# Performance work log

Measured on AMD Instinct MI355X. Metric: run time of the kernel, lower is better.

## Reference

```python
import jax, jax.numpy as jnp
import numpy as np

N, A, AD, D, H, KTOP = 5, 900, 8, 256, 8, 300


def _bbox_min_max(anchor):
    # anchor: [N,A,8] = x,y,z,logw,logl,logh,sin_yaw,cos_yaw
    xyz = anchor[..., :3]
    w, l, h = [jnp.exp(anchor[..., i]) for i in (3, 4, 5)]
    sy, cy = anchor[..., 6], anchor[..., 7]
    yaw = jnp.arctan2(sy, cy)
    ca, sa = jnp.abs(jnp.cos(yaw)), jnp.abs(jnp.sin(yaw))
    ex = 0.5 * (l * ca + w * sa)
    ey = 0.5 * (l * sa + w * ca)
    half = jnp.stack([ex, ey, 0.5 * h], axis=-1)
    return xyz - half, xyz + half


def _forward(i2j_anchor, b_anchor, b_feature, transform_matrix, anchor_embed,
             w_roi, b_roi, bn_g, bn_b, fc1_w, fc1_b, fc2_w, fc2_b,
             anc_w, anc_b, lam_w, lam_b, wq, bq, wk, bk, wv, bv, wo, bo,
             ln_g, ln_b, K):
    n, a, ad = b_anchor.shape
    d = b_feature.shape[-1]
    heads = lam_w.shape[-1]
    dh = d // heads
    # ROI scoring + topk selection of anchors to broadcast to neighbors
    roi = jax.nn.sigmoid(b_feature @ w_roi + b_roi)[..., 0]              # [N,A]
    top_scores, top_idx = jax.lax.top_k(roi, K)                          # [N,K]
    conf = top_scores > 0.5                                              # [N,K]
    nbr = jnp.take_along_axis(b_feature, top_idx[..., None], axis=1)     # [N,K,D]
    idx4 = jnp.broadcast_to(top_idx[None, :, :, None], (n, n, K, ad))
    i2j_sel = jnp.take_along_axis(i2j_anchor, idx4, axis=2)              # [N,N,K,AD]
    # remove self (eye-mask): off-diagonal j per row i, row-major order
    offdiag = np.array([[j for j in range(n) if j != i] for i in range(n)])
    rows = np.arange(n)[:, None]
    m = K * (n - 1)
    i2j_rm = i2j_sel[rows, offdiag].reshape(n, m, ad)                    # [N,M,AD]
    tm_rm = transform_matrix[rows, offdiag]                              # [N,N-1,4,4]
    key_feat = nbr[offdiag].reshape(n, m, d)                             # [N,M,D]
    conf_rm = conf[offdiag].reshape(n, m, 1)
    nf_masked = key_feat * conf_rm
    # bbox-range masked aggregation of neighbor features into ego anchors
    mn, mx = _bbox_min_max(b_anchor)                                     # [N,A,3]
    centers = i2j_rm[..., :3]                                            # [N,M,3]
    inside = jnp.all((centers[:, None, :, :] >= mn[:, :, None, :]) &
                     (centers[:, None, :, :] <= mx[:, :, None, :]), axis=-1)  # [N,A,M]
    agg = jnp.einsum('nam,nmd->nad', inside.astype(b_feature.dtype), nf_masked)
    is_greater_than_range = ~jnp.any(inside, axis=1)                     # [N,M]
    b_feature = b_feature + agg
    # transform-matrix encoding: first 3 rows of 4x4 -> BN -> MLP
    mlp_in = tm_rm[:, :, :3, :].reshape(-1, 12)
    mu = mlp_in.mean(0)
    var = mlp_in.var(0)
    xbn = (mlp_in - mu) / jnp.sqrt(var + 1e-5) * bn_g + bn_b
    t = jax.nn.relu(xbn @ fc1_w + fc1_b) @ fc2_w + fc2_b                 # [N*(N-1),D]
    trans_enc = jnp.repeat(t.reshape(n, n - 1, 1, d), K, axis=2).reshape(n, m, d)
    key_pos = i2j_rm @ anc_w + anc_b + trans_enc                         # anchorencoder + trans
    # distance-biased attention mask
    diff = b_anchor[:, :, None, :2] - i2j_rm[:, None, :, :2]
    dist = jnp.sqrt(jnp.sum(diff * diff, axis=-1) + 1e-12)               # cdist [N,A,M]
    lm = (b_feature @ lam_w + lam_b).transpose(0, 2, 1)                  # [N,H,A]
    bias = -jnp.log1p(dist)[:, None, :, :] * lm[..., None]               # [N,H,A,M]
    # multi-head attention (query=b_feature(+anchor_embed pos), key/value=neighbors)
    q = b_feature + anchor_embed
    k = key_feat + key_pos
    v = key_feat
    qh = (q @ wq + bq).reshape(n, a, heads, dh)
    kh = (k @ wk + bk).reshape(n, m, heads, dh)
    vh = (v @ wv + bv).reshape(n, m, heads, dh)
    logits = jnp.einsum('nahd,nmhd->nham', qh, kh) / np.sqrt(dh).astype(np.float32) + bias
    attn = jax.nn.softmax(logits, axis=-1)
    out = jnp.einsum('nham,nmhd->nahd', attn, vh).reshape(n, a, d) @ wo + bo
    res = b_feature + out                                                # residual (identity=query)
    mu2 = res.mean(-1, keepdims=True)
    var2 = res.var(-1, keepdims=True)
    return (res - mu2) / jnp.sqrt(var2 + 1e-5) * ln_g + ln_b


def setup_inputs() -> dict:
    key = jax.random.key(0)
    ks = jax.random.split(key, 24)
    s = 0.05
    inp = {
        'i2j_anchor': jax.random.normal(ks[0], (N, N, A, AD), jnp.float32),
        'b_anchor': jax.random.normal(ks[1], (N, A, AD), jnp.float32),
        'b_feature': jax.random.normal(ks[2], (N, A, D), jnp.float32),
        'transform_matrix': jax.random.normal(ks[3], (N, N, 4, 4), jnp.float32),
        'anchor_embed': jax.random.normal(ks[4], (N, A, D), jnp.float32),
        'w_roi': jax.random.normal(ks[5], (D, 1), jnp.float32) * s,
        'b_roi': jnp.zeros((1,), jnp.float32),
        'bn_g': jnp.ones((12,), jnp.float32),
        'bn_b': jnp.zeros((12,), jnp.float32),
        'fc1_w': jax.random.normal(ks[6], (12, D), jnp.float32) * s,
        'fc1_b': jnp.zeros((D,), jnp.float32),
        'fc2_w': jax.random.normal(ks[7], (D, D), jnp.float32) * s,
        'fc2_b': jnp.zeros((D,), jnp.float32),
        'anc_w': jax.random.normal(ks[8], (AD, D), jnp.float32) * s,
        'anc_b': jnp.zeros((D,), jnp.float32),
        'lam_w': jax.random.normal(ks[9], (D, H), jnp.float32) * s,
        'lam_b': jnp.zeros((H,), jnp.float32),
        'wq': jax.random.normal(ks[10], (D, D), jnp.float32) * s,
        'bq': jnp.zeros((D,), jnp.float32),
        'wk': jax.random.normal(ks[11], (D, D), jnp.float32) * s,
        'bk': jnp.zeros((D,), jnp.float32),
        'wv': jax.random.normal(ks[12], (D, D), jnp.float32) * s,
        'bv': jnp.zeros((D,), jnp.float32),
        'wo': jax.random.normal(ks[13], (D, D), jnp.float32) * s,
        'bo': jnp.zeros((D,), jnp.float32),
        'ln_g': jnp.ones((D,), jnp.float32),
        'ln_b': jnp.zeros((D,), jnp.float32),
        'K': KTOP,
    }
    return inp


def reference(i2j_anchor, b_anchor, b_feature, transform_matrix, anchor_embed,
              w_roi, b_roi, bn_g, bn_b, fc1_w, fc1_b, fc2_w, fc2_b,
              anc_w, anc_b, lam_w, lam_b, wq, bq, wk, bk, wv, bv, wo, bo,
              ln_g, ln_b, K):
    return _forward(i2j_anchor, b_anchor, b_feature, transform_matrix, anchor_embed,
                    w_roi, b_roi, bn_g, bn_b, fc1_w, fc1_b, fc2_w, fc2_b,
                    anc_w, anc_b, lam_w, lam_b, wq, bq, wk, bk, wv, bv, wo, bo,
                    ln_g, ln_b, K)
```

## Files before the change

### kernel.cpp

```cpp
#include <hip/hip_runtime.h>
#include <math.h>

#define N_ 5
#define A_ 900
#define AD_ 8
#define D_ 256
#define H_ 8
#define DH_ 32
#define K_ 300
#define NM1_ 4
#define M_ 1200
#define MP_ 1216
#define KC_ 64
#define HALF_ 600
#define NCHUNK2_ 10

typedef _Float16 f16x8 __attribute__((ext_vector_type(8)));
typedef _Float16 f16x4 __attribute__((ext_vector_type(4)));
typedef float f32x4 __attribute__((ext_vector_type(4)));

#define LOG2E_ 1.4426950408889634f

__global__ __launch_bounds__(256) void score_kernel(const float* __restrict__ bf,
                                                    const float* __restrict__ w,
                                                    const float* __restrict__ b,
                                                    float* __restrict__ scores) {
  int wid = threadIdx.x >> 6, lane = threadIdx.x & 63;
  int row = blockIdx.x * 4 + wid;
  if (row >= N_ * A_) return;
  const float* x = bf + (long)row * D_;
  float dot = 0.f;
#pragma unroll
  for (int t = 0; t < 4; t++) dot += x[lane + 64 * t] * w[lane + 64 * t];
#pragma unroll
  for (int o = 32; o; o >>= 1) dot += __shfl_xor(dot, o, 64);
  if (lane == 0) scores[row] = 1.0f / (1.0f + expf(-(dot + b[0])));
}

__global__ __launch_bounds__(1024) void topk_kernel(const float* __restrict__ scores,
                                                    int* __restrict__ top_idx,
                                                    float* __restrict__ conf) {
  __shared__ float sc[1024];
  __shared__ int si[1024];
  int i = blockIdx.x, t = threadIdx.x;
  sc[t] = (t < A_) ? scores[i * A_ + t] : -INFINITY;
  si[t] = t;
  __syncthreads();
  for (int k = 2; k <= 1024; k <<= 1) {
    for (int j = k >> 1; j > 0; j >>= 1) {
      int ixj = t ^ j;
      if (ixj > t) {
        bool dir = ((t & k) == 0);
        float a = sc[t], b = sc[ixj];
        bool sw = dir ? (a < b) : (a > b);
        if (sw) {
          sc[t] = b; sc[ixj] = a;
          int tmp = si[t]; si[t] = si[ixj]; si[ixj] = tmp;
        }
      }
      __syncthreads();
    }
  }
  if (t < K_) {
    top_idx[i * K_ + t] = si[t];
    conf[i * K_ + t] = sc[t] > 0.5f ? 1.0f : 0.0f;
  }
}

__global__ __launch_bounds__(256) void mlp_kernel(const float* __restrict__ tm,
                                                  const float* __restrict__ bn_g, const float* __restrict__ bn_b,
                                                  const float* __restrict__ fc1_w, const float* __restrict__ fc1_b,
                                                  const float* __restrict__ fc2_w, const float* __restrict__ fc2_b,
                                                  float* __restrict__ t_out) {
  int r = blockIdx.x;
  int t = threadIdx.x;
  __shared__ float x[20][12];
  __shared__ float y[12];
  __shared__ float hbuf[D_];
  if (t < 240) {
    int rr = t / 12, f = t % 12;
    int i = rr / NM1_, jj = rr % NM1_;
    int j = jj < i ? jj : jj + 1;
    int r4 = f / 4, c4 = f % 4;
    x[rr][f] = tm[((long)(i * N_ + j) * 4 + r4) * 4 + c4];
  }
  __syncthreads();
  if (t < 12) {
    float s = 0.f;
    for (int rr = 0; rr < 20; rr++) s += x[rr][t];
    float m = s / 20.0f;
    float v = 0.f;
    for (int rr = 0; rr < 20; rr++) { float d = x[rr][t] - m; v += d * d; }
    v /= 20.0f;
    y[t] = (x[r][t] - m) * rsqrtf(v + 1e-5f) * bn_g[t] + bn_b[t];
  }
  __syncthreads();
  float acc = fc1_b[t];
#pragma unroll
  for (int f = 0; f < 12; f++) acc += y[f] * fc1_w[f * D_ + t];
  hbuf[t] = fmaxf(acc, 0.0f);
  __syncthreads();
  float acc2 = fc2_b[t];
  for (int k = 0; k < D_; k++) acc2 += hbuf[k] * fc2_w[k * D_ + t];
  t_out[r * D_ + t] = acc2;
}

#define GKT_ 10
__global__ __launch_bounds__(256) void gather_kernel(const float* __restrict__ b_feature,
                                                     const float* __restrict__ i2j_anchor,
                                                     const int* __restrict__ top_idx,
                                                     const float* __restrict__ conf,
                                                     const float* __restrict__ anc_w,
                                                     const float* __restrict__ anc_b,
                                                     const float* __restrict__ t_mlp,
                                                     _Float16* __restrict__ key_feat16,
                                                     float* __restrict__ conf_rm,
                                                     float* __restrict__ i2j_rm,
                                                     _Float16* __restrict__ key_in16) {
  int blk = blockIdx.x;
  int i = blk / NM1_, jj = blk % NM1_;
  int j = jj < i ? jj : jj + 1;
  int k0 = blockIdx.y * GKT_;
  int c = threadIdx.x;
  __shared__ float aw[AD_][D_];
#pragma unroll
  for (int r = 0; r < AD_; r++) aw[r][c] = anc_w[r * D_ + c];
  float ab = anc_b[c];
  float tv = t_mlp[(i * NM1_ + jj) * D_ + c];
  __syncthreads();
  for (int k = k0; k < k0 + GKT_; k++) {
    int idx = top_idx[j * K_ + k];
    float cf = conf[j * K_ + k];
    const float* src = b_feature + ((long)(j * A_ + idx)) * D_;
    float val = src[c];
    long mrow = (long)i * M_ + jj * K_ + k;
    key_feat16[mrow * D_ + c] = (_Float16)val;
    const float* ap = i2j_anchor + ((long)((i * N_ + j) * A_ + idx)) * AD_;
    if (c < AD_) i2j_rm[mrow * AD_ + c] = ap[c];
    if (c == 0) conf_rm[mrow] = cf;
    float pos = ab + tv;
#pragma unroll
    for (int r = 0; r < AD_; r++) pos += ap[r] * aw[r][c];
    key_in16[mrow * D_ + c] = (_Float16)(val + pos);
  }
}

__global__ __launch_bounds__(256) void trans_kernel(const float* __restrict__ w0, const float* __restrict__ w1,
                                                    const float* __restrict__ w2, const float* __restrict__ w3,
                                                    const _Float16* __restrict__ kf,
                                                    _Float16* __restrict__ wT, _Float16* __restrict__ kT) {
  int bid = blockIdx.x;
  int t = threadIdx.x;
  if (bid < 64) {
    int y = bid >> 4, tile = bid & 15;
    const float* src = (y == 0) ? w0 : (y == 1) ? w1 : (y == 2) ? w2 : w3;
    _Float16* dst = wT + (size_t)y * D_ * D_;
    int kr = (tile >> 2) * 64, nc = (tile & 3) * 64;
    __shared__ float lds[64][65];
#pragma unroll
    for (int r = 0; r < 16; r++) {
      int row = r * 4 + (t >> 6), col = t & 63;
      lds[row][col] = src[(size_t)(kr + row) * D_ + nc + col];
    }
    __syncthreads();
#pragma unroll
    for (int r = 0; r < 16; r++) {
      int orow = r * 4 + (t >> 6), ocol = t & 63;
      dst[(size_t)(nc + orow) * D_ + kr + ocol] = (_Float16)lds[ocol][orow];
    }
  } else {
    int b = bid - 64;
    int i = b / 76, rem = b % 76;
    int m0 = (rem % 19) * 64, d0 = (rem / 19) * 64;
    __shared__ _Float16 lds2[64][66];
    const _Float16* src = kf + (size_t)i * M_ * D_;
    _Float16* dst = kT + (size_t)i * D_ * M_;
#pragma unroll
    for (int r = 0; r < 16; r++) {
      int row = r * 4 + (t >> 6), col = t & 63;
      int m = m0 + row;
      lds2[row][col] = (m < M_) ? src[(size_t)m * D_ + d0 + col] : (_Float16)0.0f;
    }
    __syncthreads();
#pragma unroll
    for (int r = 0; r < 16; r++) {
      int orow = r * 4 + (t >> 6), ocol = t & 63;
      int m = m0 + ocol;
      if (m < M_) dst[(size_t)(d0 + orow) * M_ + m] = lds2[ocol][orow];
    }
  }
}

__global__ __launch_bounds__(256) void insbias_kernel(const float* __restrict__ i2j_rm,
                                                      const float* __restrict__ conf_rm,
                                                      const float* __restrict__ ban,
                                                      _Float16* __restrict__ inside,
                                                      _Float16* __restrict__ Lbuf) {
  int i = blockIdx.x;
  int g = blockIdx.y;
  __shared__ float cx[M_], cy[M_], cz[M_], cf[M_];
  for (int m = threadIdx.x; m < M_; m += 256) {
    const float* cp = i2j_rm + ((long)i * M_ + m) * AD_;
    cx[m] = cp[0]; cy[m] = cp[1]; cz[m] = cp[2];
    cf[m] = conf_rm[(long)i * M_ + m];
  }
  __syncthreads();
#pragma unroll
  for (int r = 0; r < 4; r++) {
    int a = g * 4 + r;
    int row = i * A_ + a;
    const float* ap = ban + (long)row * AD_;
    float ax = ap[0], ay = ap[1], az = ap[2];
    float w = expf(ap[3]), l = expf(ap[4]), hh = expf(ap[5]);
    float yaw = atan2f(ap[6], ap[7]);
    float ca = fabsf(cosf(yaw)), sa = fabsf(sinf(yaw));
    float ex = 0.5f * (l * ca + w * sa);
    float ey = 0.5f * (l * sa + w * ca);
    float ez = 0.5f * hh;
    float mn0 = ax - ex, mn1 = ay - ey, mn2 = az - ez;
    float mx0 = ax + ex, mx1 = ay + ey, mx2 = az + ez;
    _Float16* ldst = Lbuf + (size_t)row * MP_;
    _Float16* idst = inside + (size_t)row * M_;
    for (int m = threadIdx.x; m < M_; m += 256) {
      float c0 = cx[m], c1 = cy[m], c2 = cz[m];
      bool ins = (c0 >= mn0) && (c0 <= mx0) && (c1 >= mn1) && (c1 <= mx1) && (c2 >= mn2) && (c2 <= mx2);
      idst[m] = ins ? (_Float16)cf[m] : (_Float16)0.0f;
      float dx = ax - c0, dy = ay - c1;
      ldst[m] = (_Float16)log1pf(sqrtf(dx * dx + dy * dy + 1e-12f));
    }
  }
}

#define GLD_ 74
template <typename TO, bool HAS_BIAS, bool HAS_RES, bool VTRANS = false>
__device__ __forceinline__ void gemm_tile_body(
    const _Float16* __restrict__ A, int lda, int Mr,
    const _Float16* __restrict__ B, int ldb,
    const float* __restrict__ bias, const float* __restrict__ res,
    TO* __restrict__ C, int ldc,
    int m0, int n0, int k_begin, int k_end) {
  __shared__ _Float16 As[64 * GLD_];
  __shared__ _Float16 Bs[64 * GLD_];
  int tid = threadIdx.x;
  int lane = tid & 63;
  int wid = tid >> 6;
  int wr = (wid >> 1) * 32, wc = (wid & 1) * 32;
  int lr = lane & 15, lk = (lane >> 4) * 8;
  int srow = tid >> 3;
  int scol = (tid & 7) * 8;
  f16x8 aR[2], bR[2];
  f16x8 zero8 = {};
  auto loadg = [&](int kb) {
#pragma unroll
    for (int r = 0; r < 2; r++) {
      int gm = m0 + srow + r * 32;
      int gk = kb + scol;
      aR[r] = (gm < Mr && gk < k_end) ? *(const f16x8*)&A[(size_t)gm * lda + gk] : zero8;
      int gn = n0 + srow + r * 32;
      bR[r] = (gk < k_end) ? *(const f16x8*)&B[(size_t)gn * ldb + gk] : zero8;
    }
  };
  auto store_lds = [&]() {
#pragma unroll
    for (int r = 0; r < 2; r++) {
      *(f16x8*)&As[(srow + r * 32) * GLD_ + scol] = aR[r];
      *(f16x8*)&Bs[(srow + r * 32) * GLD_ + scol] = bR[r];
    }
  };
  f32x4 acc[2][2] = {};
  int niter = (k_end - k_begin + 63) >> 6;
  loadg(k_begin);
  store_lds();
  __syncthreads();
  for (int it = 0; it < niter; ++it) {
    bool more = (it + 1 < niter);
    if (more) loadg(k_begin + (it + 1) * 64);
#pragma unroll
    for (int ks = 0; ks < 2; ks++) {
      f16x8 af[2], bf[2];
#pragma unroll
      for (int mi = 0; mi < 2; mi++) af[mi] = *(const f16x8*)&As[(wr + mi * 16 + lr) * GLD_ + ks * 32 + lk];
#pragma unroll
      for (int ni = 0; ni < 2; ni++) bf[ni] = *(const f16x8*)&Bs[(wc + ni * 16 + lr) * GLD_ + ks * 32 + lk];
#pragma unroll
      for (int mi = 0; mi < 2; mi++)
#pragma unroll
        for (int ni = 0; ni < 2; ni++)
          acc[mi][ni] = __builtin_amdgcn_mfma_f32_16x16x32_f16(af[mi], bf[ni], acc[mi][ni], 0, 0, 0);
    }
    __syncthreads();
    if (more) { store_lds(); __syncthreads(); }
  }
  if (VTRANS) {
#pragma unroll
    for (int mi = 0; mi < 2; mi++)
#pragma unroll
      for (int ni = 0; ni < 2; ni++)
#pragma unroll
        for (int rr = 0; rr < 4; rr++) {
          int ml = wr + mi * 16 + (lane >> 4) * 4 + rr;
          int dl = wc + ni * 16 + lr;
          float v = acc[mi][ni][rr];
          if (HAS_BIAS) v += bias[n0 + dl];
          As[dl * 72 + ml] = (_Float16)v;
        }
    __syncthreads();
    int dl = tid >> 2, mp = (tid & 3) * 16;
    int gd = n0 + dl;
#pragma unroll
    for (int e8 = 0; e8 < 2; e8++) {
      int gm = m0 + mp + e8 * 8;
      if (gm < Mr) {
        int ii = gm / M_, mm = gm - ii * M_;
        *(f16x8*)&((_Float16*)C)[(size_t)(ii * D_ + gd) * ldc + mm] =
            *(const f16x8*)&As[dl * 72 + mp + e8 * 8];
      }
    }
    return;
  }
#pragma unroll
  for (int mi = 0; mi < 2; mi++)
#pragma unroll
    for (int ni = 0; ni < 2; ni++)
#pragma unroll
      for (int rr = 0; rr < 4; rr++) {
        int row = m0 + wr + mi * 16 + (lane >> 4) * 4 + rr;
        int col = n0 + wc + ni * 16 + lr;
        if (row < Mr) {
          float v = acc[mi][ni][rr];
          if (HAS_BIAS) v += bias[col];
          if (HAS_RES) v += res[(size_t)row * ldc + col];
          C[(size_t)row * ldc + col] = (TO)v;
        }
      }
}

__global__ __launch_bounds__(256) void agg_kernel(const _Float16* __restrict__ inside16,
                                                  const _Float16* __restrict__ kT16,
                                                  float* __restrict__ partial) {
  int i = blockIdx.z >> 2, sk = blockIdx.z & 3;
  int kb = sk * 320;
  int ke = kb + 320 < M_ ? kb + 320 : M_;
  gemm_tile_body<float, false, false>(
      inside16 + (size_t)i * A_ * M_, M_, A_,
      kT16 + (size_t)i * D_ * M_, M_,
      nullptr, nullptr,
      partial + (size_t)(sk * N_ + i) * A_ * D_, D_,
      blockIdx.x * 64, blockIdx.y * 64, kb, ke);
}

__global__ __launch_bounds__(256) void agg_reduce(const float* __restrict__ partial,
                                                  const float* __restrict__ b_feature,
                                                  const float* __restrict__ anchor_embed,
                                                  const float* __restrict__ lam_w,
                                                  const float* __restrict__ lam_b,
                                                  float* __restrict__ bf_upd,
                                                  _Float16* __restrict__ qin16,
                                                  float* __restrict__ lm_rm) {
  int wid = threadIdx.x >> 6, lane = threadIdx.x & 63;
  int rg = blockIdx.x * 4 + wid;
  int d0 = lane * 4;
  float lw[4][8];
#pragma unroll
  for (int e = 0; e < 4; e++) {
#pragma unroll
    for (int h = 0; h < 8; h++) lw[e][h] = lam_w[(d0 + e) * 8 + h];
  }
  float4 s = *(const float4*)&partial[(size_t)rg * D_ + d0];
#pragma unroll
  for (int sk = 1; sk < 4; sk++) {
    float4 p = *(const float4*)&partial[((size_t)sk * N_ * A_ + rg) * D_ + d0];
    s.x += p.x; s.y += p.y; s.z += p.z; s.w += p.w;
  }
  float4 bf = *(const float4*)&b_feature[(size_t)rg * D_ + d0];
  s.x += bf.x; s.y += bf.y; s.z += bf.z; s.w += bf.w;
  *(float4*)&bf_upd[(size_t)rg * D_ + d0] = s;
  float4 ae = *(const float4*)&anchor_embed[(size_t)rg * D_ + d0];
  f16x4 q4;
  q4[0] = (_Float16)(s.x + ae.x); q4[1] = (_Float16)(s.y + ae.y);
  q4[2] = (_Float16)(s.z + ae.z); q4[3] = (_Float16)(s.w + ae.w);
  *(f16x4*)&qin16[(size_t)rg * D_ + d0] = q4;
  float sv[4] = {s.x, s.y, s.z, s.w};
  float acc[8] = {};
#pragma unroll
  for (int e = 0; e < 4; e++)
#pragma unroll
    for (int h = 0; h < 8; h++) acc[h] += sv[e] * lw[e][h];
#pragma unroll
  for (int h = 0; h < 8; h++) {
#pragma unroll
    for (int o = 32; o; o >>= 1) acc[h] += __shfl_xor(acc[h], o, 64);
  }
  if (lane == 0) {
#pragma unroll
    for (int h = 0; h < 8; h++) lm_rm[(size_t)rg * H_ + h] = acc[h] + lam_b[h];
  }
}

__global__ __launch_bounds__(256) void qkv_kernel(const _Float16* __restrict__ qA,
                                                  const _Float16* __restrict__ kA,
                                                  const _Float16* __restrict__ vA,
                                                  const _Float16* __restrict__ wT,
                                                  const float* __restrict__ bq,
                                                  const float* __restrict__ bk,
                                                  const float* __restrict__ bv,
                                                  _Float16* __restrict__ qC,
                                                  _Float16* __restrict__ kC,
                                                  _Float16* __restrict__ vT) {
  int bid = blockIdx.x;
  if (bid < 284) {
    int mt = bid % 71, nt = bid / 71;
    gemm_tile_body<_Float16, true, false>(qA, D_, 4500, wT, D_, bq, nullptr, qC, D_,
                                          mt * 64, nt * 64, 0, D_);
  } else if (bid < 660) {
    int t = bid - 284;
    int mt = t % 94, nt = t / 94;
    gemm_tile_body<_Float16, true, false>(kA, D_, 6000, wT + D_ * D_, D_, bk, nullptr, kC, D_,
                                          mt * 64, nt * 64, 0, D_);
  } else {
    int t = bid - 660;
    int mt = t % 94, nt = t / 94;
    gemm_tile_body<_Float16, true, false, true>(vA, D_, 6000, wT + 2 * D_ * D_, D_, bv, nullptr, vT, MP_,
                                                mt * 64, nt * 64, 0, D_);
  }
}

__global__ __launch_bounds__(256) void outp_kernel(const _Float16* __restrict__ att16,
                                                   const _Float16* __restrict__ woT,
                                                   float* __restrict__ partial2) {
  int bid = blockIdx.x;
  int sk = bid >= 284 ? 1 : 0;
  int t = bid - sk * 284;
  int mt = t % 71, nt = t / 71;
  gemm_tile_body<float, false, false>(att16, D_, 4500, woT, D_, nullptr, nullptr,
                                      partial2 + (size_t)sk * 4500 * D_, D_,
                                      mt * 64, nt * 64, sk * 128, sk * 128 + 128);
}

#define LQP_ 72
#define LKS_ 40
__global__ __launch_bounds__(256) void attn_mfma(const _Float16* __restrict__ qh16,
                                                 const _Float16* __restrict__ kh16,
                                                 const _Float16* __restrict__ vhT,
                                                 const float* __restrict__ lm_rm,
                                                 const _Float16* __restrict__ Lbuf,
                                                 float* __restrict__ part_ms,
                                                 float* __restrict__ part_o) {
  int bid = blockIdx.x;
  int wgid = (bid & 7) * 150 + (bid >> 3);
  int ih = wgid / 30;
  int rest = wgid % 30;
  int half = rest / 15, qt = rest % 15;
  int i = ih >> 3, h = ih & 7;
  int a0 = qt * 64;
  int mbase = half * HALF_;
  int mlimit = mbase + HALF_;

  __shared__ _Float16 QP[64 * LQP_];
  __shared__ _Float16 Ks[64 * LKS_];
  __shared__ _Float16 Vs[32 * LQP_];
  __shared__ _Float16 Ls[64 * LQP_];
  __shared__ float lmvs[64];

  int tid = threadIdx.x;
  int lane = tid & 63;
  int w16 = (tid >> 6) * 16;
  int lr = lane & 15;
  int lk = (lane >> 4) * 8;
  int mq = (lane >> 4) * 4;
  int srow = tid >> 2, spiece = tid & 3;
  int vrow = tid >> 3, vpc = (tid & 7) * 8;

  {
    int aq = a0 + srow;
    int a_ld = aq < A_ ? aq : A_ - 1;
    const uint4* src = (const uint4*)(qh16 + ((long)(i * A_ + a_ld) * D_ + h * DH_));
    *(uint4*)&QP[srow * LQP_ + spiece * 8] = src[spiece];
  }
  if (tid < 64) {
    int aq = a0 + tid;
    int a_ld = aq < A_ ? aq : A_ - 1;
    lmvs[tid] = lm_rm[(long)(i * A_ + a_ld) * H_ + h];
  }

  const _Float16* kb = kh16 + (long)i * M_ * D_ + h * DH_;
  const _Float16* vb = vhT + (size_t)(i * D_ + h * DH_) * MP_;
  const _Float16* lptr[2];
#pragma unroll
  for (int rr = 0; rr < 2; rr++) {
    int aq = a0 + vrow + rr * 32;
    int a_ld = aq < A_ ? aq : A_ - 1;
    lptr[rr] = Lbuf + (size_t)(i * A_ + a_ld) * MP_ + vpc;
  }

  uint4 kvR;
  f16x8 vvR, lR[2];
  auto loadr = [&](int c) {
    int m0 = mbase + c * KC_;
    int mrow = m0 + srow;
    kvR = (mrow < M_) ? ((const uint4*)(kb + (long)mrow * D_))[spiece] : make_uint4(0, 0, 0, 0);
    vvR = *(const f16x8*)&vb[(size_t)vrow * MP_ + m0 + vpc];
#pragma unroll
    for (int rr = 0; rr < 2; rr++) lR[rr] = *(const f16x8*)&lptr[rr][m0];
  };

  __syncthreads();

  int qrow = w16 + lr;
  float lmv2 = lmvs[qrow] * LOG2E_;
  f16x8 qa = *(const f16x8*)&QP[qrow * LQP_ + lk];

  float m_run = -INFINITY, s_part = 0.0f;
  f32x4 oacc[2] = {};

  loadr(0);

  const float SC2 = 0.17677669529663687f * LOG2E_;

  for (int c = 0; c < NCHUNK2_; c++) {
    int m0 = mbase + c * KC_;
    __syncthreads();
    *(uint4*)&Ks[srow * LKS_ + spiece * 8] = kvR;
    *(f16x8*)&Vs[vrow * LQP_ + vpc] = vvR;
#pragma unroll
    for (int rr = 0; rr < 2; rr++) *(f16x8*)&Ls[(vrow + rr * 32) * LQP_ + vpc] = lR[rr];
    if (c + 1 < NCHUNK2_) loadr(c + 1);
    __syncthreads();

    f32x4 sacc[4];
#pragma unroll
    for (int mb = 0; mb < 4; mb++) {
      f16x8 kf = *(const f16x8*)&Ks[(mb * 16 + lr) * LKS_ + lk];
      sacc[mb] = __builtin_amdgcn_mfma_f32_16x16x32_f16(kf, qa, (f32x4){0.f, 0.f, 0.f, 0.f}, 0, 0, 0);
    }

    float lg[4][4];
#pragma unroll
    for (int mb = 0; mb < 4; mb++) {
      f16x4 l4 = *(const f16x4*)&Ls[qrow * LQP_ + mb * 16 + mq];
#pragma unroll
      for (int rr = 0; rr < 4; rr++) {
        int mcol = m0 + mb * 16 + mq + rr;
        float v = sacc[mb][rr] * SC2 - (float)l4[rr] * lmv2;
        lg[mb][rr] = (mcol < mlimit) ? v : -INFINITY;
      }
    }
    float cm = -INFINITY;
#pragma unroll
    for (int mb = 0; mb < 4; mb++)
#pragma unroll
      for (int rr = 0; rr < 4; rr++) cm = fmaxf(cm, lg[mb][rr]);
    cm = fmaxf(cm, __shfl_xor(cm, 16, 64));
    cm = fmaxf(cm, __shfl_xor(cm, 32, 64));
    float nm = fmaxf(m_run, cm);
    float corr = exp2f(m_run - nm);
    m_run = nm;
    float ps = 0.0f;
#pragma unroll
    for (int mb = 0; mb < 4; mb++) {
      f16x4 p4;
#pragma unroll
      for (int rr = 0; rr < 4; rr++) {
        float p = exp2f(lg[mb][rr] - nm);
        ps += p;
        p4[rr] = (_Float16)p;
      }
      *(f16x4*)&QP[qrow * LQP_ + mb * 16 + mq] = p4;
    }
    s_part = s_part * corr + ps;
#pragma unroll
    for (int r = 0; r < 4; r++) {
      float cr = __shfl(corr, (lane & 48) + mq + r, 64);
      oacc[0][r] *= cr;
      oacc[1][r] *= cr;
    }

#pragma unroll
    for (int ks = 0; ks < 2; ks++) {
      f16x8 pa = *(const f16x8*)&QP[(w16 + lr) * LQP_ + ks * 32 + lk];
#pragma unroll
      for (int db = 0; db < 2; db++) {
        f16x8 vf = *(const f16x8*)&Vs[(db * 16 + lr) * LQP_ + ks * 32 + lk];
        oacc[db] = __builtin_amdgcn_mfma_f32_16x16x32_f16(pa, vf, oacc[db], 0, 0, 0);
      }
    }
  }

  float st = s_part;
  st += __shfl_xor(st, 16, 64);
  st += __shfl_xor(st, 32, 64);

  size_t base = (size_t)(half * 40 + ih) * A_;
  if (lane < 16) {
    int a = a0 + w16 + lane;
    if (a < A_) {
      part_ms[(base + a) * 2 + 0] = m_run;
      part_ms[(base + a) * 2 + 1] = st;
    }
  }
#pragma unroll
  for (int r = 0; r < 4; r++) {
    int a = a0 + w16 + mq + r;
    if (a < A_) {
      size_t rowb = base + a;
      part_o[rowb * 32 + lr] = oacc[0][r];
      part_o[rowb * 32 + 16 + lr] = oacc[1][r];
    }
  }
}

__global__ __launch_bounds__(256) void attn_merge(const float* __restrict__ part_ms,
                                                  const float* __restrict__ part_o,
                                                  _Float16* __restrict__ att16) {
  int t = threadIdx.x;
  int R = blockIdx.x * 8 + (t >> 5);
  int d = t & 31;
  int ih = R / A_, a = R % A_;
  int i = ih >> 3, h = ih & 7;
  size_t r0 = (size_t)ih * A_ + a;
  size_t r1 = (size_t)(40 + ih) * A_ + a;
  float m0 = part_ms[r0 * 2], s0 = part_ms[r0 * 2 + 1];
  float m1 = part_ms[r1 * 2], s1 = part_ms[r1 * 2 + 1];
  float M = fmaxf(m0, m1);
  float e0 = exp2f(m0 - M), e1 = exp2f(m1 - M);
  float inv = 1.0f / (s0 * e0 + s1 * e1);
  float o = part_o[r0 * 32 + d] * e0 + part_o[r1 * 32 + d] * e1;
  att16[((size_t)(i * A_ + a)) * D_ + h * DH_ + d] = (_Float16)(o * inv);
}

__global__ __launch_bounds__(256) void ln_kernel(const float* __restrict__ partial2,
                                                 const float* __restrict__ bo,
                                                 const float* __restrict__ resid,
                                                 const float* __restrict__ g,
                                                 const float* __restrict__ b,
                                                 float* __restrict__ out) {
  int row = blockIdx.x;
  int t = threadIdx.x;
  size_t idx = (size_t)row * D_ + t;
  float v = partial2[idx] + partial2[(size_t)4500 * D_ + idx] + bo[t] + resid[idx];
  float s = v, sq = v * v;
#pragma unroll
  for (int o = 32; o; o >>= 1) {
    s += __shfl_xor(s, o, 64);
    sq += __shfl_xor(sq, o, 64);
  }
  __shared__ float ss[4], ssq[4];
  int wid = t >> 6, lane = t & 63;
  if (lane == 0) { ss[wid] = s; ssq[wid] = sq; }
  __syncthreads();
  float ts = ss[0] + ss[1] + ss[2] + ss[3];
  float tq = ssq[0] + ssq[1] + ssq[2] + ssq[3];
  float mean = ts / (float)D_;
  float var = tq / (float)D_ - mean * mean;
  out[idx] = (v - mean) * rsqrtf(var + 1e-5f) * g[t] + b[t];
}

extern "C" void kernel_launch(void* const* d_in, const int* in_sizes, int n_in,
                              void* d_out, int out_size, void* d_ws, size_t ws_size,
                              hipStream_t stream) {
  const float* i2j_anchor   = (const float*)d_in[0];
  const float* b_anchor     = (const float*)d_in[1];
  const float* b_feature    = (const float*)d_in[2];
  const float* tm           = (const float*)d_in[3];
  const float* anchor_embed = (const float*)d_in[4];
  const float* w_roi  = (const float*)d_in[5];
  const float* b_roi  = (const float*)d_in[6];
  const float* bn_g   = (const float*)d_in[7];
  const float* bn_b   = (const float*)d_in[8];
  const float* fc1_w  = (const float*)d_in[9];
  const float* fc1_b  = (const float*)d_in[10];
  const float* fc2_w  = (const float*)d_in[11];
  const float* fc2_b  = (const float*)d_in[12];
  const float* anc_w  = (const float*)d_in[13];
  const float* anc_b  = (const float*)d_in[14];
  const float* lam_w  = (const float*)d_in[15];
  const float* lam_b  = (const float*)d_in[16];
  const float* wq = (const float*)d_in[17];
  const float* bq = (const float*)d_in[18];
  const float* wk = (const float*)d_in[19];
  const float* bk = (const float*)d_in[20];
  const float* wv = (const float*)d_in[21];
  const float* bv = (const float*)d_in[22];
  const float* wo = (const float*)d_in[23];
  const float* bo = (const float*)d_in[24];
  const float* ln_g = (const float*)d_in[25];
  const float* ln_b = (const float*)d_in[26];

  float* ws = (float*)d_ws;
  size_t off = 0;
  auto alloc = [&](size_t n) { float* p = ws + off; off += (n + 3) & ~(size_t)3; return p; };

  float* scores     = alloc(N_ * A_);
  int*   top_idx    = (int*)alloc(N_ * K_);
  float* conf       = alloc(N_ * K_);
  float* t_mlp      = alloc(20 * D_);
  float* conf_rm    = alloc((size_t)N_ * M_);
  float* i2j_rm     = alloc((size_t)N_ * M_ * AD_);
  _Float16* key_feat16 = (_Float16*)alloc((size_t)N_ * M_ * D_ / 2);
  _Float16* key_in16   = (_Float16*)alloc((size_t)N_ * M_ * D_ / 2);
  _Float16* kT16       = (_Float16*)alloc((size_t)N_ * D_ * M_ / 2);
  _Float16* inside16   = (_Float16*)alloc((size_t)N_ * A_ * M_ / 2);
  _Float16* wT16       = (_Float16*)alloc((size_t)4 * D_ * D_ / 2);
  _Float16* Lbuf16     = (_Float16*)alloc((size_t)N_ * A_ * MP_ / 2 + 16);
  float* partial    = alloc((size_t)4 * N_ * A_ * D_);
  float* bf_upd     = alloc((size_t)N_ * A_ * D_);
  _Float16* qin16   = (_Float16*)alloc((size_t)N_ * A_ * D_ / 2);
  _Float16* qh16    = (_Float16*)alloc((size_t)N_ * A_ * D_ / 2);
  _Float16* kh16    = (_Float16*)alloc((size_t)N_ * M_ * D_ / 2);
  _Float16* vhT16   = (_Float16*)alloc((size_t)N_ * D_ * MP_ / 2 + 16);
  float* lm_rm      = alloc((size_t)N_ * A_ * H_);
  _Float16* att16   = (_Float16*)alloc((size_t)N_ * A_ * D_ / 2);
  float* partial2   = alloc((size_t)2 * N_ * A_ * D_);
  float* part_ms    = alloc((size_t)2 * 40 * A_ * 2);
  float* part_o     = alloc((size_t)2 * 40 * A_ * 32);

  score_kernel<<<(N_ * A_ + 3) / 4, 256, 0, stream>>>(b_feature, w_roi, b_roi, scores);
  topk_kernel<<<N_, 1024, 0, stream>>>(scores, top_idx, conf);
  mlp_kernel<<<20, 256, 0, stream>>>(tm, bn_g, bn_b, fc1_w, fc1_b, fc2_w, fc2_b, t_mlp);
  gather_kernel<<<dim3(N_ * NM1_, K_ / GKT_), 256, 0, stream>>>(b_feature, i2j_anchor, top_idx, conf,
                                                                anc_w, anc_b, t_mlp,
                                                                key_feat16, conf_rm, i2j_rm, key_in16);
  trans_kernel<<<64 + 380, 256, 0, stream>>>(wq, wk, wv, wo, key_feat16, wT16, kT16);
  insbias_kernel<<<dim3(N_, A_ / 4), 256, 0, stream>>>(i2j_rm, conf_rm, b_anchor, inside16, Lbuf16);
  agg_kernel<<<dim3(15, 4, N_ * 4), 256, 0, stream>>>(inside16, kT16, partial);
  agg_reduce<<<(N_ * A_) / 4, 256, 0, stream>>>(partial, b_feature, anchor_embed, lam_w, lam_b,
                                                bf_upd, qin16, lm_rm);
  qkv_kernel<<<284 + 376 + 376, 256, 0, stream>>>(qin16, key_in16, key_feat16, wT16,
                                                  bq, bk, bv, qh16, kh16, vhT16);
  attn_mfma<<<1200, 256, 0, stream>>>(qh16, kh16, vhT16, lm_rm, Lbuf16, part_ms, part_o);
  attn_merge<<<(40 * A_) / 8, 256, 0, stream>>>(part_ms, part_o, att16);
  outp_kernel<<<568, 256, 0, stream>>>(att16, wT16 + 3 * D_ * D_, partial2);
  ln_kernel<<<N_ * A_, 256, 0, stream>>>(partial2, bo, bf_upd, ln_g, ln_b, (float*)d_out);
}
```

Measured before the change: 176.3 us.

## Fuse score/topk/MLP into one front kernel and add lazy softmax rescaling

Merges the ROI scoring, top-k bitonic sort and transform MLP into a single launch, so two kernel launches and the scores buffer go away. Top-k now sorts raw logits and compares them to zero instead of comparing sigmoid outputs to 0.5. The attention loop also gains lazy online-softmax rescaling: the running max and the output rescale are skipped unless some row's max grows by more than a threshold. The column-limit mask is applied only on the last chunk. The lazy rescale could risk fp16 overflow of probabilities (up to 2^11.5), and the front kernel does the scoring on only five blocks.

```diff
diff --git a/kernel.cpp b/kernel.cpp
--- a/kernel.cpp
+++ b/kernel.cpp
@@ -21,88 +21,91 @@
 
 #define LOG2E_ 1.4426950408889634f
 
-__global__ __launch_bounds__(256) void score_kernel(const float* __restrict__ bf,
-                                                    const float* __restrict__ w,
-                                                    const float* __restrict__ b,
-                                                    float* __restrict__ scores) {
-  int wid = threadIdx.x >> 6, lane = threadIdx.x & 63;
-  int row = blockIdx.x * 4 + wid;
-  if (row >= N_ * A_) return;
-  const float* x = bf + (long)row * D_;
-  float dot = 0.f;
-#pragma unroll
-  for (int t = 0; t < 4; t++) dot += x[lane + 64 * t] * w[lane + 64 * t];
-#pragma unroll
-  for (int o = 32; o; o >>= 1) dot += __shfl_xor(dot, o, 64);
-  if (lane == 0) scores[row] = 1.0f / (1.0f + expf(-(dot + b[0])));
-}
-
-__global__ __launch_bounds__(1024) void topk_kernel(const float* __restrict__ scores,
-                                                    int* __restrict__ top_idx,
-                                                    float* __restrict__ conf) {
-  __shared__ float sc[1024];
-  __shared__ int si[1024];
-  int i = blockIdx.x, t = threadIdx.x;
-  sc[t] = (t < A_) ? scores[i * A_ + t] : -INFINITY;
-  si[t] = t;
-  __syncthreads();
-  for (int k = 2; k <= 1024; k <<= 1) {
-    for (int j = k >> 1; j > 0; j >>= 1) {
-      int ixj = t ^ j;
-      if (ixj > t) {
-        bool dir = ((t & k) == 0);
-        float a = sc[t], b = sc[ixj];
-        bool sw = dir ? (a < b) : (a > b);
-        if (sw) {
-          sc[t] = b; sc[ixj] = a;
-          int tmp = si[t]; si[t] = si[ixj]; si[ixj] = tmp;
+__global__ __launch_bounds__(1024) void front_kernel(const float* __restrict__ bf,
+                                                     const float* __restrict__ w_roi,
+                                                     const float* __restrict__ b_roi,
+                                                     const float* __restrict__ tm,
+                                                     const float* __restrict__ bn_g, const float* __restrict__ bn_b,
+                                                     const float* __restrict__ fc1_w, const float* __restrict__ fc1_b,
+                                                     const float* __restrict__ fc2_w, const float* __restrict__ fc2_b,
+                                                     int* __restrict__ top_idx,
+                                                     float* __restrict__ conf,
+                                                     float* __restrict__ t_out) {
+  int t = threadIdx.x;
+  if (blockIdx.x < N_) {
+    int i = blockIdx.x;
+    __shared__ float sc[1024];
+    __shared__ int si[1024];
+    __shared__ float wv[D_];
+    if (t < D_) wv[t] = w_roi[t];
+    sc[t] = -INFINITY;
+    si[t] = t;
+    __syncthreads();
+    int wid = t >> 6, lane = t & 63;
+    for (int row = wid; row < A_; row += 16) {
+      const float* x = bf + ((size_t)i * A_ + row) * D_;
+      float dot = 0.f;
+#pragma unroll
+      for (int e = 0; e < 4; e++) dot += x[lane + 64 * e] * wv[lane + 64 * e];
+#pragma unroll
+      for (int o = 32; o; o >>= 1) dot += __shfl_xor(dot, o, 64);
+      if (lane == 0) sc[row] = dot + b_roi[0];
+    }
+    __syncthreads();
+    for (int k = 2; k <= 1024; k <<= 1) {
+      for (int j = k >> 1; j > 0; j >>= 1) {
+        int ixj = t ^ j;
+        if (ixj > t) {
+          bool dir = ((t & k) == 0);
+          float a = sc[t], b = sc[ixj];
+          bool sw = dir ? (a < b) : (a > b);
+          if (sw) {
+            sc[t] = b; sc[ixj] = a;
+            int tmp = si[t]; si[t] = si[ixj]; si[ixj] = tmp;
+          }
         }
+        __syncthreads();
       }
-      __syncthreads();
-    }
-  }
-  if (t < K_) {
-    top_idx[i * K_ + t] = si[t];
-    conf[i * K_ + t] = sc[t] > 0.5f ? 1.0f : 0.0f;
-  }
-}
-
-__global__ __launch_bounds__(256) void mlp_kernel(const float* __restrict__ tm,
-                                                  const float* __restrict__ bn_g, const float* __restrict__ bn_b,
-                                                  const float* __restrict__ fc1_w, const float* __restrict__ fc1_b,
-                                                  const float* __restrict__ fc2_w, const float* __restrict__ fc2_b,
-                                                  float* __restrict__ t_out) {
-  int r = blockIdx.x;
-  int t = threadIdx.x;
-  __shared__ float x[20][12];
-  __shared__ float y[12];
-  __shared__ float hbuf[D_];
-  if (t < 240) {
-    int rr = t / 12, f = t % 12;
-    int i = rr / NM1_, jj = rr % NM1_;
-    int j = jj < i ? jj : jj + 1;
-    int r4 = f / 4, c4 = f % 4;
-    x[rr][f] = tm[((long)(i * N_ + j) * 4 + r4) * 4 + c4];
-  }
-  __syncthreads();
-  if (t < 12) {
-    float s = 0.f;
-    for (int rr = 0; rr < 20; rr++) s += x[rr][t];
-    float m = s / 20.0f;
-    float v = 0.f;
-    for (int rr = 0; rr < 20; rr++) { float d = x[rr][t] - m; v += d * d; }
-    v /= 20.0f;
-    y[t] = (x[r][t] - m) * rsqrtf(v + 1e-5f) * bn_g[t] + bn_b[t];
-  }
-  __syncthreads();
-  float acc = fc1_b[t];
-#pragma unroll
-  for (int f = 0; f < 12; f++) acc += y[f] * fc1_w[f * D_ + t];
-  hbuf[t] = fmaxf(acc, 0.0f);
-  __syncthreads();
-  float acc2 = fc2_b[t];
-  for (int k = 0; k < D_; k++) acc2 += hbuf[k] * fc2_w[k * D_ + t];
-  t_out[r * D_ + t] = acc2;
+    }
+    if (t < K_) {
+      top_idx[i * K_ + t] = si[t];
+      conf[i * K_ + t] = sc[t] > 0.0f ? 1.0f : 0.0f;
+    }
+  } else {
+    int r = blockIdx.x - N_;
+    __shared__ float x2[20][12];
+    __shared__ float y2[12];
+    __shared__ float hbuf[D_];
+    if (t < 240) {
+      int rr = t / 12, f = t % 12;
+      int i = rr / NM1_, jj = rr % NM1_;
+      int j = jj < i ? jj : jj + 1;
+      x2[rr][f] = tm[((long)(i * N_ + j) * 4 + (f / 4)) * 4 + (f % 4)];
+    }
+    __syncthreads();
+    if (t < 12) {
+      float s = 0.f;
+      for (int rr = 0; rr < 20; rr++) s += x2[rr][t];
+      float m = s / 20.0f;
+      float v = 0.f;
+      for (int rr = 0; rr < 20; rr++) { float d = x2[rr][t] - m; v += d * d; }
+      v /= 20.0f;
+      y2[t] = (x2[r][t] - m) * rsqrtf(v + 1e-5f) * bn_g[t] + bn_b[t];
+    }
+    __syncthreads();
+    if (t < D_) {
+      float acc = fc1_b[t];
+#pragma unroll
+      for (int f = 0; f < 12; f++) acc += y2[f] * fc1_w[f * D_ + t];
+      hbuf[t] = fmaxf(acc, 0.0f);
+    }
+    __syncthreads();
+    if (t < D_) {
+      float acc2 = fc2_b[t];
+      for (int k = 0; k < D_; k++) acc2 += hbuf[k] * fc2_w[k * D_ + t];
+      t_out[r * D_ + t] = acc2;
+    }
+  }
 }
 
 #define GKT_ 10
@@ -439,6 +442,7 @@
 
 #define LQP_ 72
 #define LKS_ 40
+#define THR2_ 11.5f
 __global__ __launch_bounds__(256) void attn_mfma(const _Float16* __restrict__ qh16,
                                                  const _Float16* __restrict__ kh16,
                                                  const _Float16* __restrict__ vhT,
@@ -517,7 +521,7 @@
 
   const float SC2 = 0.17677669529663687f * LOG2E_;
 
-  for (int c = 0; c < NCHUNK2_; c++) {
+  auto chunk_body = [&](int c, bool masked) {
     int m0 = mbase + c * KC_;
     __syncthreads();
     *(uint4*)&Ks[srow * LKS_ + spiece * 8] = kvR;
@@ -540,9 +544,12 @@
       f16x4 l4 = *(const f16x4*)&Ls[qrow * LQP_ + mb * 16 + mq];
 #pragma unroll
       for (int rr = 0; rr < 4; rr++) {
-        int mcol = m0 + mb * 16 + mq + rr;
         float v = sacc[mb][rr] * SC2 - (float)l4[rr] * lmv2;
-        lg[mb][rr] = (mcol < mlimit) ? v : -INFINITY;
+        if (masked) {
+          int mcol = m0 + mb * 16 + mq + rr;
+          v = (mcol < mlimit) ? v : -INFINITY;
+        }
+        lg[mb][rr] = v;
       }
     }
     float cm = -INFINITY;
@@ -552,27 +559,34 @@
       for (int rr = 0; rr < 4; rr++) cm = fmaxf(cm, lg[mb][rr]);
     cm = fmaxf(cm, __shfl_xor(cm, 16, 64));
     cm = fmaxf(cm, __shfl_xor(cm, 32, 64));
-    float nm = fmaxf(m_run, cm);
-    float corr = exp2f(m_run - nm);
-    m_run = nm;
+
+    bool upd = !__all(cm - m_run <= THR2_);
+    float corr = 1.0f;
+    if (upd) {
+      float nm = fmaxf(m_run, cm);
+      corr = exp2f(m_run - nm);
+      m_run = nm;
+      lmvs[qrow] = corr;
+    }
     float ps = 0.0f;
 #pragma unroll
     for (int mb = 0; mb < 4; mb++) {
       f16x4 p4;
 #pragma unroll
       for (int rr = 0; rr < 4; rr++) {
-        float p = exp2f(lg[mb][rr] - nm);
+        float p = exp2f(lg[mb][rr] - m_run);
         ps += p;
         p4[rr] = (_Float16)p;
       }
       *(f16x4*)&QP[qrow * LQP_ + mb * 16 + mq] = p4;
     }
-    s_part = s_part * corr + ps;
-#pragma unroll
-    for (int r = 0; r < 4; r++) {
-      float cr = __shfl(corr, (lane & 48) + mq + r, 64);
-      oacc[0][r] *= cr;
-      oacc[1][r] *= cr;
+    if (upd) {
+      float4 c4 = *(const float4*)&lmvs[w16 + mq];
+      s_part = s_part * corr + ps;
+      oacc[0][0] *= c4.x; oacc[0][1] *= c4.y; oacc[0][2] *= c4.z; oacc[0][3] *= c4.w;
+      oacc[1][0] *= c4.x; oacc[1][1] *= c4.y; oacc[1][2] *= c4.z; oacc[1][3] *= c4.w;
+    } else {
+      s_part += ps;
     }
 
 #pragma unroll
@@ -584,7 +598,10 @@
         oacc[db] = __builtin_amdgcn_mfma_f32_16x16x32_f16(pa, vf, oacc[db], 0, 0, 0);
       }
     }
-  }
+  };
+
+  for (int c = 0; c < NCHUNK2_ - 1; c++) chunk_body(c, false);
+  chunk_body(NCHUNK2_ - 1, true);
 
   float st = s_part;
   st += __shfl_xor(st, 16, 64);
@@ -690,7 +707,6 @@
   size_t off = 0;
   auto alloc = [&](size_t n) { float* p = ws + off; off += (n + 3) & ~(size_t)3; return p; };
 
-  float* scores     = alloc(N_ * A_);
   int*   top_idx    = (int*)alloc(N_ * K_);
   float* conf       = alloc(N_ * K_);
   float* t_mlp      = alloc(20 * D_);
@@ -714,9 +730,9 @@
   float* part_ms    = alloc((size_t)2 * 40 * A_ * 2);
   float* part_o     = alloc((size_t)2 * 40 * A_ * 32);
 
-  score_kernel<<<(N_ * A_ + 3) / 4, 256, 0, stream>>>(b_feature, w_roi, b_roi, scores);
-  topk_kernel<<<N_, 1024, 0, stream>>>(scores, top_idx, conf);
-  mlp_kernel<<<20, 256, 0, stream>>>(tm, bn_g, bn_b, fc1_w, fc1_b, fc2_w, fc2_b, t_mlp);
+  front_kernel<<<N_ + 20, 1024, 0, stream>>>(b_feature, w_roi, b_roi, tm,
+                                             bn_g, bn_b, fc1_w, fc1_b, fc2_w, fc2_b,
+                                             top_idx, conf, t_mlp);
   gather_kernel<<<dim3(N_ * NM1_, K_ / GKT_), 256, 0, stream>>>(b_feature, i2j_anchor, top_idx, conf,
                                                                 anc_w, anc_b, t_mlp,
                                                                 key_feat16, conf_rm, i2j_rm, key_in16);
```

Measured after the change: 185.9 us. 1.05x slower.
